# Kernel optimization log

Measured on AMD Instinct MI355X. Metric: run time of the kernel, lower is better.

Reference implementation:

```python
import jax, jax.numpy as jnp
import numpy as np

R = 8
TOP_K_A = 2
TOP_K_B = 2
SCALING = 16.0 / R  # lora_alpha / r


def setup_inputs() -> dict:
    key = jax.random.key(0)
    k1, k2, k3, k4, k5 = jax.random.split(key, 5)
    B, S, D_IN, D_OUT, EA, EB = 4, 2048, 4096, 4096, 8, 8
    x = jax.random.normal(k1, (B, S, D_IN), dtype=jnp.float32)
    router_logits_a = jax.random.normal(k2, (B * S, EA), dtype=jnp.float32)
    router_logits_b = jax.random.normal(k3, (B * S, EB), dtype=jnp.float32)
    # nn.Linear(in, r).weight -> [r, in]; stacked per expert: [E_a, r, in]
    Wa = jax.random.normal(k4, (EA, R, D_IN), dtype=jnp.float32) * (1.0 / np.sqrt(D_IN))
    # nn.Linear(r, out).weight -> [out, r]; stacked: [E_b, out, r]
    Wb = jax.random.normal(k5, (EB, D_OUT, R), dtype=jnp.float32) * (1.0 / np.sqrt(R))
    return {"x": x, "router_logits_a": router_logits_a,
            "router_logits_b": router_logits_b, "Wa": Wa, "Wb": Wb}


def reference(x, router_logits_a, router_logits_b, Wa, Wb):
    B, S, D_IN = x.shape
    flat_x = x.reshape(-1, D_IN)  # [T, D_in]

    # --- A experts: dense compute over all experts, then top-k gather ---
    topk_logits_a, topk_idx_a = jax.lax.top_k(router_logits_a, TOP_K_A)
    weights_a = jax.nn.softmax(topk_logits_a, axis=-1)  # [T, k_a]
    a_all = jnp.einsum('ti,eri->ter', flat_x, Wa)  # [T, E_a, r]
    sel_a = jnp.take_along_axis(a_all, topk_idx_a[:, :, None], axis=1)  # [T, k_a, r]
    mid = jnp.sum(sel_a * weights_a[:, :, None], axis=1)  # [T, r]

    # --- B experts: dense compute over all experts, then top-k gather ---
    b_all = jnp.einsum('tr,eor->teo', mid, Wb)  # [T, E_b, D_out]
    topk_logits_b, topk_idx_b = jax.lax.top_k(router_logits_b, TOP_K_B)
    weights_b = jax.nn.softmax(topk_logits_b, axis=-1)  # [T, k_b]
    sel_b = jnp.take_along_axis(b_all, topk_idx_b[:, :, None], axis=1)  # [T, k_b, D_out]
    out_flat = jnp.sum(sel_b * weights_b[:, :, None], axis=1) * SCALING  # [T, D_out]
    output = out_flat.reshape(B, S, -1)

    # --- load-balancing aux losses (torch.var is unbiased) ---
    probs_a = jnp.mean(jax.nn.softmax(router_logits_a, axis=-1), axis=0)
    probs_b = jnp.mean(jax.nn.softmax(router_logits_b, axis=-1), axis=0)
    aux_loss_a = Wa.shape[0] * jnp.var(probs_a, ddof=1)
    aux_loss_b = Wb.shape[0] * jnp.var(probs_b, ddof=1)
    return output, aux_loss_a, aux_loss_b
```

## Files before the change

kernel.cpp:

```cpp
#include <hip/hip_runtime.h>

#define T_TOK 8192
#define D_IN  4096
#define D_OUT 4096

typedef _Float16 h2 __attribute__((ext_vector_type(2)));
typedef _Float16 h4 __attribute__((ext_vector_type(4)));
typedef _Float16 h8 __attribute__((ext_vector_type(8)));
typedef float    f4v __attribute__((ext_vector_type(4)));

__device__ __forceinline__ h2 pkrtz(float a, float b) {
    auto r = __builtin_amdgcn_cvt_pkrtz(a, b);
    h2 o; __builtin_memcpy(&o, &r, 4); return o;
}
__device__ __forceinline__ h8 cvt8(float4 f0, float4 f1) {
    h2 p0 = pkrtz(f0.x, f0.y), p1 = pkrtz(f0.z, f0.w);
    h2 p2 = pkrtz(f1.x, f1.y), p3 = pkrtz(f1.z, f1.w);
    return (h8){p0.x, p0.y, p1.x, p1.y, p2.x, p2.y, p3.x, p3.y};
}
__device__ __forceinline__ h8 as_h8(uint4 u) { h8 b; __builtin_memcpy(&b, &u, 16); return b; }

__device__ __forceinline__ void gl_lds16(const void* g, void* l) {
    __builtin_amdgcn_global_load_lds(
        (const __attribute__((address_space(1))) unsigned int*)g,
        (__attribute__((address_space(3))) unsigned int*)l, 16, 0, 0);
}


__global__ __launch_bounds__(256)
void prep(const float* __restrict__ Wa, const float* __restrict__ Wb,
          const float* __restrict__ la, const float* __restrict__ lb,
          _Float16* __restrict__ WaB, _Float16* __restrict__ WbB,
          double* __restrict__ pax) {
    const int bid = blockIdx.x, tx = threadIdx.x;
    __shared__ double red[4][16];
    if (bid < 256) {
        int gid = bid * 256 + tx;
        int er = gid >> 10, k0 = (gid & 1023) * 4;
        float4 v = ((const float4*)Wa)[gid];
        h2 p0 = pkrtz(v.x, v.y), p1 = pkrtz(v.z, v.w);
        h4 o = { p0.x, p0.y, p1.x, p1.y };
        int it = k0 >> 7, ks = (k0 >> 5) & 3, kf = (k0 >> 3) & 3;
        int g = er >> 4, mr = er & 15;
        *(h4*)(WaB + it * 8192 + (ks * 4 + g) * 512 + (kf * 16 + mr) * 8
               + (k0 & 7)) = o;
    } else if (bid < 384) {
        int gid = (bid - 256) * 256 + tx;
        int e = gid >> 12, o = gid & 4095;
        const float4* p = (const float4*)(Wb + ((size_t)e * 4096 + o) * 8);
        h8 v = cvt8(p[0], p[1]);
        int ch = o >> 7, wv = (o >> 4) & 7, mr = o & 15;
        *(h8*)(WbB + (size_t)ch * 8192 + ((e >> 2) * 8 + wv) * 512
               + ((e & 3) * 16 + mr) * 8) = v;
    } else {
        const int ab = bid - 384;
        const int t = ab * 256 + tx;
        double loc[16];
        {
            float l[8];
#pragma unroll
            for (int i = 0; i < 8; ++i) l[i] = la[(size_t)t * 8 + i];
            float m = l[0];
#pragma unroll
            for (int i = 1; i < 8; ++i) m = fmaxf(m, l[i]);
            float s = 0.f, e[8];
#pragma unroll
            for (int i = 0; i < 8; ++i) { e[i] = __expf(l[i] - m); s += e[i]; }
#pragma unroll
            for (int i = 0; i < 8; ++i) loc[i] = (double)(e[i] / s);
        }
        {
            float l[8];
#pragma unroll
            for (int i = 0; i < 8; ++i) l[i] = lb[(size_t)t * 8 + i];
            float m = l[0];
#pragma unroll
            for (int i = 1; i < 8; ++i) m = fmaxf(m, l[i]);
            float s = 0.f, e[8];
#pragma unroll
            for (int i = 0; i < 8; ++i) { e[i] = __expf(l[i] - m); s += e[i]; }
#pragma unroll
            for (int i = 0; i < 8; ++i) loc[8 + i] = (double)(e[i] / s);
        }
        const int lane = tx & 63, wid = tx >> 6;
#pragma unroll
        for (int v = 0; v < 16; ++v) {
            double s = loc[v];
#pragma unroll
            for (int off = 32; off > 0; off >>= 1) s += __shfl_down(s, off, 64);
            if (lane == 0) red[wid][v] = s;
        }
        __syncthreads();
        if (tx < 16)
            pax[ab * 16 + tx] = red[0][tx] + red[1][tx] + red[2][tx] + red[3][tx];
    }
}

__global__ __launch_bounds__(512, 4)
void fused(const float* __restrict__ x, const _Float16* __restrict__ WaB,
           const _Float16* __restrict__ WbB, const float* __restrict__ la,
           const float* __restrict__ lb, float* __restrict__ out,
           const double* __restrict__ pax) {
    __shared__ char S[73728];
    __shared__ float sW0[16], sW1[16], sCb[16][8];
    __shared__ int   sE0[16], sE1[16];
    __shared__ double sl[16];

    const int tx = threadIdx.x, l = tx & 63, w = tx >> 6;
    const int mr = l & 15, kf = l >> 4;
    const int m0 = blockIdx.x * 16;
    const int g  = w & 3;
    const int kh = w >> 2;
    const int er1 = g * 16 + mr;
    float* pLp = (float*)S;
    _Float16* MbLp = (_Float16*)(S + 8448);

    f4v acc = (f4v){0.f, 0.f, 0.f, 0.f};

#define STAGE1(IT, BUF) do {                                                   \
    _Pragma("unroll") for (int i_ = 0; i_ < 3; ++i_) {                         \
        int p_ = w * 3 + i_;                                                   \
        if (p_ < 8) {                                                          \
            const char* src_ = (const char*)x + (size_t)(m0 + mr) * 16384      \
                + (size_t)(IT) * 512 + (p_ >> 1) * 128 + kf * 32 + (p_ & 1) * 16; \
            gl_lds16(src_, S + (BUF) * 24576 + p_ * 1024);                     \
        } else {                                                               \
            int q_ = p_ - 8;                                                   \
            const char* src_ = (const char*)WaB + (size_t)(IT) * 16384         \
                + q_ * 1024 + l * 16;                                          \
            gl_lds16(src_, S + (BUF) * 24576 + 8192 + q_ * 1024);              \
        }                                                                      \
    }                                                                          \
  } while (0)

#define CMP1(BUF) do {                                                         \
    _Pragma("unroll") for (int i_ = 0; i_ < 2; ++i_) {                         \
        int ks_ = kh * 2 + i_;                                                 \
        float4 f0_ = *(const float4*)(S + (BUF) * 24576 + (ks_ * 2) * 1024 + l * 16);     \
        float4 f1_ = *(const float4*)(S + (BUF) * 24576 + (ks_ * 2 + 1) * 1024 + l * 16); \
        h8 a_ = cvt8(f0_, f1_);                                                \
        h8 b_ = *(const h8*)(S + (BUF) * 24576 + 8192                          \
                             + (ks_ * 4 + g) * 1024 + l * 16);                 \
        acc = __builtin_amdgcn_mfma_f32_16x16x32_f16(a_, b_, acc, 0, 0, 0);    \
    }                                                                          \
  } while (0)

    STAGE1(0, 0);
    STAGE1(1, 1);
    {
        int bc = 0;
        int bs = 2;
#pragma unroll 1
        for (int it = 0; it < 31; ++it) {
            asm volatile("s_waitcnt vmcnt(3)" ::: "memory");
            __builtin_amdgcn_s_barrier();
            if (it < 30) STAGE1(it + 2, bs);
            CMP1(bc);
            bc = (bc == 2) ? 0 : bc + 1;
            bs = (bs == 2) ? 0 : bs + 1;
        }
        asm volatile("s_waitcnt vmcnt(0)" ::: "memory");
        __builtin_amdgcn_s_barrier();
        CMP1(1);
    }
#undef STAGE1
#undef CMP1

#pragma unroll
    for (int r = 0; r < 4; ++r) pLp[kh * 1056 + (kf * 4 + r) * 66 + er1] = acc[r];
    __syncthreads();

    if (tx < 16) {
        const int t = tx;
        float lg[8];
#pragma unroll
        for (int i = 0; i < 8; ++i) lg[i] = la[(size_t)(m0 + t) * 8 + i];
        int e0 = 0; float b0 = lg[0];
#pragma unroll
        for (int i = 1; i < 8; ++i) if (lg[i] > b0) { b0 = lg[i]; e0 = i; }
        int e1 = -1; float b1 = -1e30f;
#pragma unroll
        for (int i = 0; i < 8; ++i) if (i != e0 && lg[i] > b1) { b1 = lg[i]; e1 = i; }
        float w1 = __expf(b1 - b0), s = 1.f + w1;
        sW0[t] = 1.f / s; sW1[t] = w1 / s; sE0[t] = e0; sE1[t] = e1;

#pragma unroll
        for (int i = 0; i < 8; ++i) lg[i] = lb[(size_t)(m0 + t) * 8 + i];
        int f0 = 0; float c0 = lg[0];
#pragma unroll
        for (int i = 1; i < 8; ++i) if (lg[i] > c0) { c0 = lg[i]; f0 = i; }
        int f1 = -1; float c1 = -1e30f;
#pragma unroll
        for (int i = 0; i < 8; ++i) if (i != f0 && lg[i] > c1) { c1 = lg[i]; f1 = i; }
        float wb1 = __expf(c1 - c0), sb = 1.f + wb1;
        float wb0s = 2.f / sb, wb1s = 2.f * wb1 / sb;
#pragma unroll
        for (int e = 0; e < 8; ++e)
            sCb[t][e] = (e == f0) ? wb0s : (e == f1) ? wb1s : 0.f;
    }
    __syncthreads();

    if (tx < 256) {
        const int t = tx >> 4, gg = tx & 15;
        const float w0 = sW0[t], w1 = sW1[t];
        const int e0 = sE0[t], e1 = sE1[t];
        const float cb = sCb[t][gg >> 1];
        h4 o;
#pragma unroll
        for (int j = 0; j < 4; ++j) {
            int r = (gg * 4 + j) & 7;
            float mid = w0 * (pLp[t * 66 + e0 * 8 + r] + pLp[1056 + t * 66 + e0 * 8 + r])
                      + w1 * (pLp[t * 66 + e1 * 8 + r] + pLp[1056 + t * 66 + e1 * 8 + r]);
            o[j] = (_Float16)(cb * mid);
        }
        *(h4*)(MbLp + ((gg >> 1) * 16 + t) * 8 + (gg & 1) * 4) = o;
    }
    __syncthreads();

    h8 a30 = *(const h8*)(MbLp + ((0 * 4 + kf) * 16 + mr) * 8);
    h8 a31 = *(const h8*)(MbLp + ((1 * 4 + kf) * 16 + mr) * 8);
    const uint4* wb4 = (const uint4*)WbB;
    float* outp = out + (size_t)(m0 + kf * 4) * D_OUT;

    uint4 C0[2], C1[2];
#define LDB3(Cd, CH) do {                                                      \
    Cd[0] = wb4[(size_t)(CH) * 1024 + w * 64 + l];                             \
    Cd[1] = wb4[(size_t)(CH) * 1024 + 512 + w * 64 + l];                       \
  } while (0)

#define CMP3(Cs, CH) do {                                                      \
    f4v o0 = (f4v){0.f,0.f,0.f,0.f};                                           \
    o0 = __builtin_amdgcn_mfma_f32_16x16x32_f16(a30, as_h8(Cs[0]), o0, 0,0,0); \
    o0 = __builtin_amdgcn_mfma_f32_16x16x32_f16(a31, as_h8(Cs[1]), o0, 0,0,0); \
    int n0_ = (CH) * 128 + w * 16 + mr;                                        \
    _Pragma("unroll") for (int r_ = 0; r_ < 4; ++r_)                           \
        outp[(size_t)r_ * D_OUT + n0_] = o0[r_];                               \
  } while (0)

    LDB3(C0, 0);
#pragma unroll 1
    for (int c = 0; c < 30; c += 2) {
        LDB3(C1, c + 1); CMP3(C0, c);
        LDB3(C0, c + 2); CMP3(C1, c + 1);
    }
    LDB3(C1, 31); CMP3(C0, 30); CMP3(C1, 31);
#undef LDB3
#undef CMP3

    if (blockIdx.x == 0) {
        if (tx < 16) {
            double s = 0.0;
#pragma unroll
            for (int b = 0; b < 32; ++b) s += pax[b * 16 + tx];
            sl[tx] = s;
        }
        __syncthreads();
        if (tx == 0) {
            double pa[8], pb[8], ma = 0.0, mb = 0.0;
            for (int e = 0; e < 8; ++e) { pa[e] = sl[e] / 8192.0;     ma += pa[e] / 8.0; }
            for (int e = 0; e < 8; ++e) { pb[e] = sl[8 + e] / 8192.0; mb += pb[e] / 8.0; }
            double va = 0.0, vb = 0.0;
            for (int e = 0; e < 8; ++e) { double d = pa[e] - ma; va += d * d; }
            for (int e = 0; e < 8; ++e) { double d = pb[e] - mb; vb += d * d; }
            out[(size_t)T_TOK * D_OUT + 0] = (float)(8.0 * va / 7.0);
            out[(size_t)T_TOK * D_OUT + 1] = (float)(8.0 * vb / 7.0);
        }
    }
}

extern "C" void kernel_launch(void* const* d_in, const int* in_sizes, int n_in,
                              void* d_out, int out_size, void* d_ws, size_t ws_size,
                              hipStream_t stream) {
    const float* x  = (const float*)d_in[0];
    const float* la = (const float*)d_in[1];
    const float* lb = (const float*)d_in[2];
    const float* Wa = (const float*)d_in[3];
    const float* Wb = (const float*)d_in[4];
    float* out = (float*)d_out;

    char* ws = (char*)d_ws;
    _Float16* WaB = (_Float16*)ws;
    _Float16* WbB = (_Float16*)(ws + 524288);
    double*   pax = (double*)(ws + 1048576);

    prep<<<416, 256, 0, stream>>>(Wa, Wb, la, lb, WaB, WbB, pax);
    fused<<<512, 512, 0, stream>>>(x, WaB, WbB, la, lb, out, pax);
}
```

Baseline: 271.0 us.

## Split fused kernel into split-K down-projection and separate up-projection kernel

Replaces the single fused kernel with two. The first kernel splits the D_in reduction into two halves across blockIdx.y, giving 1024 blocks, and writes partial rank-64 results to workspace. The second kernel uses 2048 smaller blocks: it sums the partials, applies routing, and computes the output projection, with each block covering 32 tokens and a slice of output columns so each Wb fragment feeds two MFMAs. The goal is more parallelism and better occupancy for both phases. The cost is an extra launch and a workspace round trip for the partials.

```diff
diff --git a/kernel.cpp b/kernel.cpp
--- a/kernel.cpp
+++ b/kernel.cpp
@@ -97,23 +97,15 @@
 }
 
 __global__ __launch_bounds__(512, 4)
-void fused(const float* __restrict__ x, const _Float16* __restrict__ WaB,
-           const _Float16* __restrict__ WbB, const float* __restrict__ la,
-           const float* __restrict__ lb, float* __restrict__ out,
-           const double* __restrict__ pax) {
+void g1(const float* __restrict__ x, const _Float16* __restrict__ WaB,
+        float* __restrict__ part) {
     __shared__ char S[73728];
-    __shared__ float sW0[16], sW1[16], sCb[16][8];
-    __shared__ int   sE0[16], sE1[16];
-    __shared__ double sl[16];
-
     const int tx = threadIdx.x, l = tx & 63, w = tx >> 6;
     const int mr = l & 15, kf = l >> 4;
     const int m0 = blockIdx.x * 16;
-    const int g  = w & 3;
-    const int kh = w >> 2;
+    const int y  = blockIdx.y;
+    const int g = w & 3, kh = w >> 2;
     const int er1 = g * 16 + mr;
-    float* pLp = (float*)S;
-    _Float16* MbLp = (_Float16*)(S + 8448);
 
     f4v acc = (f4v){0.f, 0.f, 0.f, 0.f};
 
@@ -122,12 +114,13 @@
         int p_ = w * 3 + i_;                                                   \
         if (p_ < 8) {                                                          \
             const char* src_ = (const char*)x + (size_t)(m0 + mr) * 16384      \
-                + (size_t)(IT) * 512 + (p_ >> 1) * 128 + kf * 32 + (p_ & 1) * 16; \
+                + (size_t)y * 8192 + (size_t)(IT) * 512                        \
+                + (p_ >> 1) * 128 + kf * 32 + (p_ & 1) * 16;                   \
             gl_lds16(src_, S + (BUF) * 24576 + p_ * 1024);                     \
         } else {                                                               \
             int q_ = p_ - 8;                                                   \
-            const char* src_ = (const char*)WaB + (size_t)(IT) * 16384         \
-                + q_ * 1024 + l * 16;                                          \
+            const char* src_ = (const char*)WaB                                \
+                + ((size_t)y * 16 + (IT)) * 16384 + q_ * 1024 + l * 16;        \
             gl_lds16(src_, S + (BUF) * 24576 + 8192 + q_ * 1024);              \
         }                                                                      \
     }                                                                          \
@@ -151,30 +144,67 @@
         int bc = 0;
         int bs = 2;
 #pragma unroll 1
-        for (int it = 0; it < 31; ++it) {
+        for (int it = 0; it < 15; ++it) {
             asm volatile("s_waitcnt vmcnt(3)" ::: "memory");
             __builtin_amdgcn_s_barrier();
-            if (it < 30) STAGE1(it + 2, bs);
+            if (it < 14) STAGE1(it + 2, bs);
             CMP1(bc);
             bc = (bc == 2) ? 0 : bc + 1;
             bs = (bs == 2) ? 0 : bs + 1;
         }
         asm volatile("s_waitcnt vmcnt(0)" ::: "memory");
         __builtin_amdgcn_s_barrier();
-        CMP1(1);
+        CMP1(0);
     }
 #undef STAGE1
 #undef CMP1
 
+    float* pLp = (float*)(S + 24576);
 #pragma unroll
     for (int r = 0; r < 4; ++r) pLp[kh * 1056 + (kf * 4 + r) * 66 + er1] = acc[r];
     __syncthreads();
-
-    if (tx < 16) {
+#pragma unroll
+    for (int rep = 0; rep < 2; ++rep) {
+        int idx = rep * 512 + tx;
+        int t = idx >> 6, er = idx & 63;
+        part[((size_t)(m0 + t) * 2 + y) * 64 + er]
+            = pLp[t * 66 + er] + pLp[1056 + t * 66 + er];
+    }
+}
+
+__global__ __launch_bounds__(256)
+void g2(const float* __restrict__ part, const _Float16* __restrict__ WbB,
+        const float* __restrict__ la, const float* __restrict__ lb,
+        float* __restrict__ out, const double* __restrict__ pax) {
+    __shared__ float    Ssum[32][68];
+    __shared__ _Float16 MbL[32 * 72];
+    __shared__ float sW0[32], sW1[32], sCb[32][8];
+    __shared__ int   sE0[32], sE1[32];
+    __shared__ double sl[16];
+
+    const int tx = threadIdx.x, l = tx & 63, w = tx >> 6;
+    const int mr = l & 15, kf = l >> 4;
+    const int bid = blockIdx.x;
+    const int tb = bid >> 3, cs = bid & 7;
+    const int t0 = tb * 32;
+
+    {
+        const float4* P4 = (const float4*)part;
+#pragma unroll
+        for (int rep = 0; rep < 2; ++rep) {
+            int idx = rep * 256 + tx;
+            int t = idx >> 4, q = idx & 15;
+            float4 a = P4[(size_t)(t0 + t) * 32 + q];
+            float4 b = P4[(size_t)(t0 + t) * 32 + 16 + q];
+            float4 s = { a.x + b.x, a.y + b.y, a.z + b.z, a.w + b.w };
+            *(float4*)&Ssum[t][q * 4] = s;
+        }
+    }
+    if (tx < 32) {
         const int t = tx;
         float lg[8];
 #pragma unroll
-        for (int i = 0; i < 8; ++i) lg[i] = la[(size_t)(m0 + t) * 8 + i];
+        for (int i = 0; i < 8; ++i) lg[i] = la[(size_t)(t0 + t) * 8 + i];
         int e0 = 0; float b0 = lg[0];
 #pragma unroll
         for (int i = 1; i < 8; ++i) if (lg[i] > b0) { b0 = lg[i]; e0 = i; }
@@ -185,7 +215,7 @@
         sW0[t] = 1.f / s; sW1[t] = w1 / s; sE0[t] = e0; sE1[t] = e1;
 
 #pragma unroll
-        for (int i = 0; i < 8; ++i) lg[i] = lb[(size_t)(m0 + t) * 8 + i];
+        for (int i = 0; i < 8; ++i) lg[i] = lb[(size_t)(t0 + t) * 8 + i];
         int f0 = 0; float c0 = lg[0];
 #pragma unroll
         for (int i = 1; i < 8; ++i) if (lg[i] > c0) { c0 = lg[i]; f0 = i; }
@@ -200,54 +230,54 @@
     }
     __syncthreads();
 
-    if (tx < 256) {
-        const int t = tx >> 4, gg = tx & 15;
-        const float w0 = sW0[t], w1 = sW1[t];
-        const int e0 = sE0[t], e1 = sE1[t];
-        const float cb = sCb[t][gg >> 1];
-        h4 o;
-#pragma unroll
-        for (int j = 0; j < 4; ++j) {
-            int r = (gg * 4 + j) & 7;
-            float mid = w0 * (pLp[t * 66 + e0 * 8 + r] + pLp[1056 + t * 66 + e0 * 8 + r])
-                      + w1 * (pLp[t * 66 + e1 * 8 + r] + pLp[1056 + t * 66 + e1 * 8 + r]);
-            o[j] = (_Float16)(cb * mid);
-        }
-        *(h4*)(MbLp + ((gg >> 1) * 16 + t) * 8 + (gg & 1) * 4) = o;
+#pragma unroll
+    for (int rep = 0; rep < 8; ++rep) {
+        int idx = rep * 256 + tx;
+        int t = idx >> 6, er = idx & 63;
+        float mid = sW0[t] * Ssum[t][sE0[t] * 8 + (er & 7)]
+                  + sW1[t] * Ssum[t][sE1[t] * 8 + (er & 7)];
+        MbL[t * 72 + er] = (_Float16)(sCb[t][er >> 3] * mid);
     }
     __syncthreads();
 
-    h8 a30 = *(const h8*)(MbLp + ((0 * 4 + kf) * 16 + mr) * 8);
-    h8 a31 = *(const h8*)(MbLp + ((1 * 4 + kf) * 16 + mr) * 8);
+    h8 a00 = *(const h8*)(MbL + (0 * 16 + mr) * 72 + 0 * 32 + kf * 8);
+    h8 a01 = *(const h8*)(MbL + (0 * 16 + mr) * 72 + 1 * 32 + kf * 8);
+    h8 a10 = *(const h8*)(MbL + (1 * 16 + mr) * 72 + 0 * 32 + kf * 8);
+    h8 a11 = *(const h8*)(MbL + (1 * 16 + mr) * 72 + 1 * 32 + kf * 8);
     const uint4* wb4 = (const uint4*)WbB;
-    float* outp = out + (size_t)(m0 + kf * 4) * D_OUT;
+    const int ch = cs * 4 + w;
+    const size_t cb = (size_t)ch * 1024;
+    float* outp = out + (size_t)(t0 + kf * 4) * D_OUT;
 
     uint4 C0[2], C1[2];
-#define LDB3(Cd, CH) do {                                                      \
-    Cd[0] = wb4[(size_t)(CH) * 1024 + w * 64 + l];                             \
-    Cd[1] = wb4[(size_t)(CH) * 1024 + 512 + w * 64 + l];                       \
+#define LDB(Cd, c) do {                                                        \
+    Cd[0] = wb4[cb + (size_t)(c) * 64 + l];                                    \
+    Cd[1] = wb4[cb + 512 + (size_t)(c) * 64 + l];                              \
   } while (0)
 
-#define CMP3(Cs, CH) do {                                                      \
-    f4v o0 = (f4v){0.f,0.f,0.f,0.f};                                           \
-    o0 = __builtin_amdgcn_mfma_f32_16x16x32_f16(a30, as_h8(Cs[0]), o0, 0,0,0); \
-    o0 = __builtin_amdgcn_mfma_f32_16x16x32_f16(a31, as_h8(Cs[1]), o0, 0,0,0); \
-    int n0_ = (CH) * 128 + w * 16 + mr;                                        \
-    _Pragma("unroll") for (int r_ = 0; r_ < 4; ++r_)                           \
-        outp[(size_t)r_ * D_OUT + n0_] = o0[r_];                               \
+#define CMP(Cs, c) do {                                                        \
+    f4v o0 = (f4v){0.f,0.f,0.f,0.f}, o1 = (f4v){0.f,0.f,0.f,0.f};              \
+    o0 = __builtin_amdgcn_mfma_f32_16x16x32_f16(a00, as_h8(Cs[0]), o0, 0,0,0); \
+    o0 = __builtin_amdgcn_mfma_f32_16x16x32_f16(a01, as_h8(Cs[1]), o0, 0,0,0); \
+    o1 = __builtin_amdgcn_mfma_f32_16x16x32_f16(a10, as_h8(Cs[0]), o1, 0,0,0); \
+    o1 = __builtin_amdgcn_mfma_f32_16x16x32_f16(a11, as_h8(Cs[1]), o1, 0,0,0); \
+    int n0 = ch * 128 + (c) * 16 + mr;                                         \
+    _Pragma("unroll") for (int r_ = 0; r_ < 4; ++r_) {                         \
+        outp[(size_t)r_ * D_OUT + n0]        = o0[r_];                         \
+        outp[(size_t)(16 + r_) * D_OUT + n0] = o1[r_]; }                       \
   } while (0)
 
-    LDB3(C0, 0);
+    LDB(C0, 0);
 #pragma unroll 1
-    for (int c = 0; c < 30; c += 2) {
-        LDB3(C1, c + 1); CMP3(C0, c);
-        LDB3(C0, c + 2); CMP3(C1, c + 1);
-    }
-    LDB3(C1, 31); CMP3(C0, 30); CMP3(C1, 31);
-#undef LDB3
-#undef CMP3
-
-    if (blockIdx.x == 0) {
+    for (int c = 0; c < 6; c += 2) {
+        LDB(C1, c + 1); CMP(C0, c);
+        LDB(C0, c + 2); CMP(C1, c + 1);
+    }
+    LDB(C1, 7); CMP(C0, 6); CMP(C1, 7);
+#undef LDB
+#undef CMP
+
+    if (bid == 0) {
         if (tx < 16) {
             double s = 0.0;
 #pragma unroll
@@ -279,10 +309,12 @@
     float* out = (float*)d_out;
 
     char* ws = (char*)d_ws;
-    _Float16* WaB = (_Float16*)ws;
-    _Float16* WbB = (_Float16*)(ws + 524288);
-    double*   pax = (double*)(ws + 1048576);
+    _Float16* WaB  = (_Float16*)ws;
+    _Float16* WbB  = (_Float16*)(ws + 524288);
+    double*   pax  = (double*)(ws + 1048576);
+    float*    partb = (float*)(ws + 1052672);
 
     prep<<<416, 256, 0, stream>>>(Wa, Wb, la, lb, WaB, WbB, pax);
-    fused<<<512, 512, 0, stream>>>(x, WaB, WbB, la, lb, out, pax);
-}
+    g1<<<dim3(512, 2), 512, 0, stream>>>(x, WaB, partb);
+    g2<<<2048, 256, 0, stream>>>(partb, WbB, la, lb, out, pax);
+}
```

New measurement: 268.5 us. Within noise of the previous version (-0.9%).
